# Kernel tuning notes

Measured on AMD Instinct MI355X. Metric: run time of the kernel, lower is better.

Reference implementation:

```python
import jax, jax.numpy as jnp
import numpy as np

BLOCK = 8
WIN = 3
PAD = WIN - 1


def _dct_mat(b, dtype):
    # Orthonormal DCT-II matrix: D[k, n] = s_k * sqrt(2/b) * cos(pi*(2n+1)k/(2b))
    n = np.arange(b)
    k = n[:, None]
    D = np.sqrt(2.0 / b) * np.cos(np.pi * (2 * n[None, :] + 1) * k / (2 * b))
    D[0, :] *= 1.0 / np.sqrt(2.0)
    return jnp.asarray(D, dtype=dtype)


def setup_inputs() -> dict:
    key = jax.random.key(0)
    k1, k2 = jax.random.split(key)
    x = jax.random.normal(k1, (8, 64, 256, 256), dtype=jnp.float32)
    conv_w = jax.random.normal(k2, (64, 64, WIN), dtype=jnp.float32) * 0.05
    conv_b = jnp.zeros((64,), dtype=jnp.float32)
    return {"x": x, "conv_w": conv_w, "conv_b": conv_b}


def reference(x, conv_w, conv_b):
    b = BLOCK
    bsz, ch, H, W = x.shape
    nH, nW = H // b, W // b
    n = nH * nW
    D = _dct_mat(b, x.dtype)

    # blockify: (bsz, ch, n_blocks, b, b)
    blk = x.reshape(bsz, ch, nH, b, nW, b).transpose(0, 1, 2, 4, 3, 5)
    blk = blk.reshape(bsz, ch, n, b, b)

    # block 2D DCT: D @ X @ D^T
    coef = jnp.einsum('kn,bcxnm,lm->bcxkl', D, blk, D)
    coef = coef.reshape(bsz, ch, n, b * b)

    # FreqConv: causal-right-padded Conv1d over the b*b frequency axis
    y = coef.transpose(0, 2, 1, 3).reshape(bsz * n, ch, b * b)
    y = jnp.pad(y, ((0, 0), (0, 0), (0, PAD)))
    y = jax.lax.conv_general_dilated(
        y, conv_w, window_strides=(1,), padding=[(0, 0)],
        dimension_numbers=('NCH', 'OIH', 'NCH'), feature_group_count=1)
    y = y + conv_b[None, :, None]
    out_ch = y.shape[1]
    y = y.reshape(bsz, n, out_ch, b * b).transpose(0, 2, 1, 3)

    # block 2D IDCT: D^T @ X @ D
    y = y.reshape(bsz, out_ch, n, b, b)
    img = jnp.einsum('kn,bcxkl,lm->bcxnm', D, y, D)

    # deblockify back to (bsz, out_ch, H, W)
    img = img.reshape(bsz, out_ch, nH, nW, b, b).transpose(0, 1, 2, 4, 3, 5)
    return img.reshape(bsz, out_ch, H, W)
```

## Files before the change

### kernel.cpp

```cpp
#include <hip/hip_runtime.h>


#define THREADS 256
#define HW 256
#define CH 64
#define CT_ROW 72
#define CT_SAMPLE (66 * CT_ROW)
#define LDS_BYTES (4 * CT_SAMPLE * 2)

typedef __attribute__((ext_vector_type(8))) short short8b;
typedef __attribute__((ext_vector_type(8))) unsigned short us8;
typedef __attribute__((ext_vector_type(4))) float f32x4;
typedef __attribute__((ext_vector_type(4))) unsigned short us4;

__device__ inline unsigned short f2bf(float f) {
    unsigned u = __builtin_bit_cast(unsigned, f);
    u += 0x7FFFu + ((u >> 16) & 1u);
    return (unsigned short)(u >> 16);
}

__device__ __constant__ static const float D8[8][8] = {
  { 0.3535533906f, 0.3535533906f, 0.3535533906f, 0.3535533906f, 0.3535533906f, 0.3535533906f, 0.3535533906f, 0.3535533906f },
  { 0.4903926402f, 0.4157348062f, 0.2777851165f, 0.0975451610f,-0.0975451610f,-0.2777851165f,-0.4157348062f,-0.4903926402f },
  { 0.4619397663f, 0.1913417162f,-0.1913417162f,-0.4619397663f,-0.4619397663f,-0.1913417162f, 0.1913417162f, 0.4619397663f },
  { 0.4157348062f,-0.0975451610f,-0.4903926402f,-0.2777851165f, 0.2777851165f, 0.4903926402f, 0.0975451610f,-0.4157348062f },
  { 0.3535533906f,-0.3535533906f,-0.3535533906f, 0.3535533906f, 0.3535533906f,-0.3535533906f,-0.3535533906f, 0.3535533906f },
  { 0.2777851165f,-0.4903926402f, 0.0975451610f, 0.4157348062f,-0.4157348062f,-0.0975451610f, 0.4903926402f,-0.2777851165f },
  { 0.1913417162f,-0.4619397663f, 0.4619397663f,-0.1913417162f,-0.1913417162f, 0.4619397663f,-0.4619397663f, 0.1913417162f },
  { 0.0975451610f,-0.2777851165f, 0.4157348062f,-0.4903926402f, 0.4903926402f,-0.4157348062f, 0.2777851165f,-0.0975451610f },
};

__global__ __launch_bounds__(256)
void prep_kernel(const float* __restrict__ conv_w, unsigned short* __restrict__ ws16) {
    int j = blockIdx.x * 256 + threadIdx.x;
    if (j < 4096) {
        int t = j >> 6, s = j & 63;
        ws16[j] = f2bf(D8[t >> 3][s >> 3] * D8[t & 7][s & 7]);
    } else if (j < 8192) {
        int jj = j - 4096;
        int s = jj >> 6, t = jj & 63;
        ws16[j] = f2bf(D8[t >> 3][s >> 3] * D8[t & 7][s & 7]);
    } else if (j < 20480) {
        int jj = j - 8192;
        int w = jj >> 12, rem = jj & 4095, o = rem >> 6, i = rem & 63;
        ws16[j] = f2bf(conv_w[o * 192 + i * 3 + w]);
    }
}

__global__ __launch_bounds__(THREADS, 4)
void dct_freq_conv_kernel(const float* __restrict__ x,
                          const unsigned short* __restrict__ ws16,
                          const float* __restrict__ conv_b,
                          float* __restrict__ out)
{
    extern __shared__ char smem[];
    unsigned short* Ct = (unsigned short*)smem;
    const unsigned short* Trm = ws16;
    const unsigned short* Urm = ws16 + 4096;
    const unsigned short* Wt  = ws16 + 8192;

    const int tid  = threadIdx.x;
    const int wid  = tid >> 6;
    const int lane = tid & 63;
    const int lr   = lane & 15;
    const int lq   = lane >> 4;
    const int bz   = blockIdx.z;
    const int by   = blockIdx.y;
    const int bxs  = blockIdx.x * 4 + wid;

    unsigned short* CtP = Ct + wid * CT_SAMPLE;

    if (lane < 36) *(us4*)&CtP[64 * CT_ROW + lane * 4] = (us4){0, 0, 0, 0};

    float bias[4];
    #pragma unroll
    for (int m = 0; m < 4; ++m) bias[m] = conv_b[m * 16 + lr];

    #pragma unroll
    for (int mg = 0; mg < 2; ++mg) {
        f32x4 acc[2][4];
        #pragma unroll
        for (int i = 0; i < 2; ++i)
            #pragma unroll
            for (int n = 0; n < 4; ++n) acc[i][n] = (f32x4){0.f, 0.f, 0.f, 0.f};

        #pragma unroll
        for (int kc = 0; kc < 2; ++kc) {
            short8b a[2], b[4];
            #pragma unroll
            for (int mh = 0; mh < 2; ++mh) {
                const int c = (mg * 2 + mh) * 16 + lr;
                const float* xp = x + (((size_t)bz * CH + c) * HW + by * 8 + kc * 4 + lq) * HW
                                    + bxs * 8;
                float4 u0 = *(const float4*)xp;
                float4 u1 = *(const float4*)(xp + 4);
                us8 pa;
                pa[0] = f2bf(u0.x); pa[1] = f2bf(u0.y); pa[2] = f2bf(u0.z); pa[3] = f2bf(u0.w);
                pa[4] = f2bf(u1.x); pa[5] = f2bf(u1.y); pa[6] = f2bf(u1.z); pa[7] = f2bf(u1.w);
                a[mh] = __builtin_bit_cast(short8b, pa);
            }
            #pragma unroll
            for (int n = 0; n < 4; ++n)
                b[n] = *(const short8b*)&Trm[(n * 16 + lr) * 64 + kc * 32 + lq * 8];
            #pragma unroll
            for (int mh = 0; mh < 2; ++mh)
                #pragma unroll
                for (int n = 0; n < 4; ++n)
                    acc[mh][n] = __builtin_amdgcn_mfma_f32_16x16x32_bf16(
                        a[mh], b[n], acc[mh][n], 0, 0, 0);
        }
        #pragma unroll
        for (int mh = 0; mh < 2; ++mh) {
            const int c0 = (mg * 2 + mh) * 16 + lq * 4;
            #pragma unroll
            for (int n = 0; n < 4; ++n) {
                us4 pk;
                #pragma unroll
                for (int j = 0; j < 4; ++j) pk[j] = f2bf(acc[mh][n][j]);
                *(us4*)&CtP[(n * 16 + lr) * CT_ROW + c0] = pk;
            }
        }
    }

    f32x4 acc2[4][4];
    #pragma unroll
    for (int n = 0; n < 4; ++n)
        #pragma unroll
        for (int m = 0; m < 4; ++m) acc2[n][m] = (f32x4){0.f, 0.f, 0.f, 0.f};

    #pragma unroll 2
    for (int kc = 0; kc < 6; ++kc) {
        const int w  = kc >> 1;
        const int i0 = (kc & 1) * 32 + 8 * lq;
        short8b a[4], b[4];
        #pragma unroll
        for (int n = 0; n < 4; ++n)
            a[n] = *(const short8b*)&CtP[(n * 16 + lr + w) * CT_ROW + i0];
        #pragma unroll
        for (int m = 0; m < 4; ++m)
            b[m] = *(const short8b*)&Wt[(w * 64 + m * 16 + lr) * 64 + i0];
        #pragma unroll
        for (int n = 0; n < 4; ++n)
            #pragma unroll
            for (int m = 0; m < 4; ++m)
                acc2[n][m] = __builtin_amdgcn_mfma_f32_16x16x32_bf16(
                    a[n], b[m], acc2[n][m], 0, 0, 0);
    }
    #pragma unroll
    for (int n = 0; n < 4; ++n) {
        const int t0 = n * 16 + 4 * lq;
        #pragma unroll
        for (int m = 0; m < 4; ++m) {
            const int o = m * 16 + lr;
            us4 pk;
            #pragma unroll
            for (int j = 0; j < 4; ++j) pk[j] = f2bf(acc2[n][m][j] + bias[m]);
            *(us4*)&CtP[o * CT_ROW + t0] = pk;
        }
    }

    #pragma unroll
    for (int mg = 0; mg < 2; ++mg) {
        f32x4 acc[2][4];
        #pragma unroll
        for (int i = 0; i < 2; ++i)
            #pragma unroll
            for (int ct = 0; ct < 4; ++ct) acc[i][ct] = (f32x4){0.f, 0.f, 0.f, 0.f};

        #pragma unroll
        for (int kc = 0; kc < 2; ++kc) {
            short8b a[2], b[4];
            #pragma unroll
            for (int mh = 0; mh < 2; ++mh)
                a[mh] = *(const short8b*)&Urm[((mg * 2 + mh) * 16 + lr) * 64 + kc * 32 + lq * 8];
            #pragma unroll
            for (int ct = 0; ct < 4; ++ct)
                b[ct] = *(const short8b*)&CtP[(ct * 16 + lr) * CT_ROW + kc * 32 + lq * 8];
            #pragma unroll
            for (int mh = 0; mh < 2; ++mh)
                #pragma unroll
                for (int ct = 0; ct < 4; ++ct)
                    acc[mh][ct] = __builtin_amdgcn_mfma_f32_16x16x32_bf16(
                        a[mh], b[ct], acc[mh][ct], 0, 0, 0);
        }
        #pragma unroll
        for (int mh = 0; mh < 2; ++mh) {
            const int s0 = (mg * 2 + mh) * 16 + lq * 4;
            const int n  = s0 >> 3;
            const int m0 = s0 & 7;
            #pragma unroll
            for (int ct = 0; ct < 4; ++ct) {
                const int o = ct * 16 + lr;
                float4 st = make_float4(acc[mh][ct][0], acc[mh][ct][1],
                                        acc[mh][ct][2], acc[mh][ct][3]);
                *(float4*)(out + (((size_t)bz * CH + o) * HW + by * 8 + n) * HW
                           + bxs * 8 + m0) = st;
            }
        }
    }
}

extern "C" void kernel_launch(void* const* d_in, const int* in_sizes, int n_in,
                              void* d_out, int out_size, void* d_ws, size_t ws_size,
                              hipStream_t stream) {
    const float* x  = (const float*)d_in[0];
    const float* cw = (const float*)d_in[1];
    const float* cb = (const float*)d_in[2];
    float* o        = (float*)d_out;
    unsigned short* ws16 = (unsigned short*)d_ws;

    prep_kernel<<<dim3(80), dim3(256), 0, stream>>>(cw, ws16);

    hipFuncSetAttribute(reinterpret_cast<const void*>(dct_freq_conv_kernel),
                        hipFuncAttributeMaxDynamicSharedMemorySize,
                        (int)LDS_BYTES);
    dim3 grid(8, 32, 8);
    dct_freq_conv_kernel<<<grid, dim3(THREADS), LDS_BYTES, stream>>>(x, ws16, cb, o);
}
```

Before: 286.0 us.

## Stage input and output through swizzled LDS for coalesced global access

Input tiles are now loaded cooperatively by the whole block as coalesced float4 rows, converted to bf16 and written into an XOR-swizzled LDS buffer before the forward DCT GEMM. Outputs pass through LDS so each store writes contiguous 32-float row segments instead of scattered 8-float pieces per wave. The weight matrices are pre-permuted into MFMA fragment order so each lane does one contiguous load. In exchange the kernel uses more LDS, adds several block-wide barriers, and lowers the occupancy hint from 4 to 3.

```diff
diff --git a/kernel.cpp b/kernel.cpp
--- a/kernel.cpp
+++ b/kernel.cpp
@@ -6,10 +6,10 @@
 #define CH 64
 #define CT_ROW 72
 #define CT_SAMPLE (66 * CT_ROW)
-#define LDS_BYTES (4 * CT_SAMPLE * 2)
+#define XB_SH 8192
+#define LDS_BYTES ((XB_SH + 4 * CT_SAMPLE) * 2)
 
 typedef __attribute__((ext_vector_type(8))) short short8b;
-typedef __attribute__((ext_vector_type(8))) unsigned short us8;
 typedef __attribute__((ext_vector_type(4))) float f32x4;
 typedef __attribute__((ext_vector_type(4))) unsigned short us4;
 
@@ -32,42 +32,44 @@
 
 __global__ __launch_bounds__(256)
 void prep_kernel(const float* __restrict__ conv_w, unsigned short* __restrict__ ws16) {
-    int j = blockIdx.x * 256 + threadIdx.x;
-    if (j < 4096) {
-        int t = j >> 6, s = j & 63;
-        ws16[j] = f2bf(D8[t >> 3][s >> 3] * D8[t & 7][s & 7]);
-    } else if (j < 8192) {
-        int jj = j - 4096;
-        int s = jj >> 6, t = jj & 63;
-        ws16[j] = f2bf(D8[t >> 3][s >> 3] * D8[t & 7][s & 7]);
-    } else if (j < 20480) {
-        int jj = j - 8192;
-        int w = jj >> 12, rem = jj & 4095, o = rem >> 6, i = rem & 63;
-        ws16[j] = f2bf(conv_w[o * 192 + i * 3 + w]);
+    int idx = blockIdx.x * 256 + threadIdx.x;
+    int j = idx & 7, lane = (idx >> 3) & 63;
+    int lrr = lane & 15, lqq = lane >> 4;
+    if (idx < 4096) {
+        int nk = idx >> 9, n = nk >> 1, kc = nk & 1;
+        int t = n * 16 + lrr, s = kc * 32 + lqq * 8 + j;
+        ws16[idx] = f2bf(D8[t >> 3][s >> 3] * D8[t & 7][s & 7]);
+    } else if (idx < 8192) {
+        int i2 = idx - 4096;
+        int mk = i2 >> 9, m = mk >> 1, kc = mk & 1;
+        int s = m * 16 + lrr, t = kc * 32 + lqq * 8 + j;
+        ws16[idx] = f2bf(D8[t >> 3][s >> 3] * D8[t & 7][s & 7]);
+    } else if (idx < 20480) {
+        int i3 = idx - 8192;
+        int grp = i3 >> 9, m = grp & 3, hc = (grp >> 2) & 1, w = grp >> 3;
+        int o = m * 16 + lrr, i = hc * 32 + lqq * 8 + j;
+        ws16[idx] = f2bf(conv_w[o * 192 + i * 3 + w]);
     }
 }
 
-__global__ __launch_bounds__(THREADS, 4)
+__global__ __launch_bounds__(THREADS, 3)
 void dct_freq_conv_kernel(const float* __restrict__ x,
                           const unsigned short* __restrict__ ws16,
                           const float* __restrict__ conv_b,
                           float* __restrict__ out)
 {
     extern __shared__ char smem[];
-    unsigned short* Ct = (unsigned short*)smem;
-    const unsigned short* Trm = ws16;
-    const unsigned short* Urm = ws16 + 4096;
-    const unsigned short* Wt  = ws16 + 8192;
-
-    const int tid  = threadIdx.x;
-    const int wid  = tid >> 6;
-    const int lane = tid & 63;
-    const int lr   = lane & 15;
-    const int lq   = lane >> 4;
-    const int bz   = blockIdx.z;
-    const int by   = blockIdx.y;
-    const int bxs  = blockIdx.x * 4 + wid;
-
+    unsigned short* Xb = (unsigned short*)smem;
+    float*          Ou = (float*)smem;
+    unsigned short* Ct = (unsigned short*)smem + XB_SH;
+    const unsigned short* Tf = ws16;
+    const unsigned short* Uf = ws16 + 4096;
+    const unsigned short* Wf = ws16 + 8192;
+
+    const int tid = threadIdx.x;
+    const int wid = tid >> 6, lane = tid & 63;
+    const int lr = lane & 15, lq = lane >> 4;
+    const int bz = blockIdx.z, by = blockIdx.y, bx = blockIdx.x;
     unsigned short* CtP = Ct + wid * CT_SAMPLE;
 
     if (lane < 36) *(us4*)&CtP[64 * CT_ROW + lane * 4] = (us4){0, 0, 0, 0};
@@ -76,51 +78,60 @@
     #pragma unroll
     for (int m = 0; m < 4; ++m) bias[m] = conv_b[m * 16 + lr];
 
-    #pragma unroll
-    for (int mg = 0; mg < 2; ++mg) {
-        f32x4 acc[2][4];
-        #pragma unroll
-        for (int i = 0; i < 2; ++i)
-            #pragma unroll
-            for (int n = 0; n < 4; ++n) acc[i][n] = (f32x4){0.f, 0.f, 0.f, 0.f};
-
-        #pragma unroll
-        for (int kc = 0; kc < 2; ++kc) {
-            short8b a[2], b[4];
-            #pragma unroll
-            for (int mh = 0; mh < 2; ++mh) {
-                const int c = (mg * 2 + mh) * 16 + lr;
-                const float* xp = x + (((size_t)bz * CH + c) * HW + by * 8 + kc * 4 + lq) * HW
-                                    + bxs * 8;
-                float4 u0 = *(const float4*)xp;
-                float4 u1 = *(const float4*)(xp + 4);
-                us8 pa;
-                pa[0] = f2bf(u0.x); pa[1] = f2bf(u0.y); pa[2] = f2bf(u0.z); pa[3] = f2bf(u0.w);
-                pa[4] = f2bf(u1.x); pa[5] = f2bf(u1.y); pa[6] = f2bf(u1.z); pa[7] = f2bf(u1.w);
-                a[mh] = __builtin_bit_cast(short8b, pa);
-            }
+    auto stage = [&](int h) {
+        #pragma unroll
+        for (int rep = 0; rep < 8; ++rep) {
+            int f4 = rep * 256 + tid;
+            int cl = f4 & 7, rl = (f4 >> 3) & 3, c = f4 >> 5;
+            const float* gp = x + ((size_t)(bz * 64 + c) * 256 + by * 8 + h * 4 + rl) * 256
+                                + bx * 32 + cl * 4;
+            float4 v = *(const float4*)gp;
+            us4 pk; pk[0] = f2bf(v.x); pk[1] = f2bf(v.y); pk[2] = f2bf(v.z); pk[3] = f2bf(v.w);
+            int smp = cl >> 1, kk = rl * 8 + (cl & 1) * 4;
+            *(us4*)&Xb[smp * 2048 + c * 32 + (kk ^ ((c & 3) << 3))] = pk;
+        }
+    };
+
+    f32x4 acc[4][4];
+    #pragma unroll
+    for (int m = 0; m < 4; ++m)
+        #pragma unroll
+        for (int n = 0; n < 4; ++n) acc[m][n] = (f32x4){0.f, 0.f, 0.f, 0.f};
+
+    auto gemm1_step = [&](int kc) {
+        short8b a[4], b[4];
+        #pragma unroll
+        for (int m = 0; m < 4; ++m) {
+            const int cA = m * 16 + lr;
+            a[m] = *(const short8b*)&Xb[wid * 2048 + cA * 32 + ((lq * 8) ^ ((cA & 3) << 3))];
+        }
+        #pragma unroll
+        for (int n = 0; n < 4; ++n)
+            b[n] = *(const short8b*)&Tf[((n * 2 + kc) * 64 + lane) * 8];
+        #pragma unroll
+        for (int m = 0; m < 4; ++m)
             #pragma unroll
             for (int n = 0; n < 4; ++n)
-                b[n] = *(const short8b*)&Trm[(n * 16 + lr) * 64 + kc * 32 + lq * 8];
-            #pragma unroll
-            for (int mh = 0; mh < 2; ++mh)
-                #pragma unroll
-                for (int n = 0; n < 4; ++n)
-                    acc[mh][n] = __builtin_amdgcn_mfma_f32_16x16x32_bf16(
-                        a[mh], b[n], acc[mh][n], 0, 0, 0);
-        }
-        #pragma unroll
-        for (int mh = 0; mh < 2; ++mh) {
-            const int c0 = (mg * 2 + mh) * 16 + lq * 4;
-            #pragma unroll
-            for (int n = 0; n < 4; ++n) {
-                us4 pk;
-                #pragma unroll
-                for (int j = 0; j < 4; ++j) pk[j] = f2bf(acc[mh][n][j]);
-                *(us4*)&CtP[(n * 16 + lr) * CT_ROW + c0] = pk;
-            }
-        }
-    }
+                acc[m][n] = __builtin_amdgcn_mfma_f32_16x16x32_bf16(a[m], b[n], acc[m][n], 0, 0, 0);
+    };
+
+    stage(0);
+    __syncthreads();
+    gemm1_step(0);
+    __syncthreads();
+    stage(1);
+    __syncthreads();
+    gemm1_step(1);
+
+    #pragma unroll
+    for (int m = 0; m < 4; ++m)
+        #pragma unroll
+        for (int n = 0; n < 4; ++n) {
+            us4 pk;
+            #pragma unroll
+            for (int j = 0; j < 4; ++j) pk[j] = f2bf(acc[m][n][j]);
+            *(us4*)&CtP[(n * 16 + lr) * CT_ROW + m * 16 + lq * 4] = pk;
+        }
 
     f32x4 acc2[4][4];
     #pragma unroll
@@ -128,74 +139,75 @@
         #pragma unroll
         for (int m = 0; m < 4; ++m) acc2[n][m] = (f32x4){0.f, 0.f, 0.f, 0.f};
 
-    #pragma unroll 2
+    #pragma unroll
     for (int kc = 0; kc < 6; ++kc) {
         const int w  = kc >> 1;
-        const int i0 = (kc & 1) * 32 + 8 * lq;
+        const int i0 = (kc & 1) * 32 + lq * 8;
         short8b a[4], b[4];
         #pragma unroll
         for (int n = 0; n < 4; ++n)
             a[n] = *(const short8b*)&CtP[(n * 16 + lr + w) * CT_ROW + i0];
         #pragma unroll
         for (int m = 0; m < 4; ++m)
-            b[m] = *(const short8b*)&Wt[(w * 64 + m * 16 + lr) * 64 + i0];
+            b[m] = *(const short8b*)&Wf[((kc * 4 + m) * 64 + lane) * 8];
         #pragma unroll
         for (int n = 0; n < 4; ++n)
             #pragma unroll
             for (int m = 0; m < 4; ++m)
-                acc2[n][m] = __builtin_amdgcn_mfma_f32_16x16x32_bf16(
-                    a[n], b[m], acc2[n][m], 0, 0, 0);
+                acc2[n][m] = __builtin_amdgcn_mfma_f32_16x16x32_bf16(a[n], b[m], acc2[n][m], 0, 0, 0);
     }
     #pragma unroll
-    for (int n = 0; n < 4; ++n) {
-        const int t0 = n * 16 + 4 * lq;
+    for (int n = 0; n < 4; ++n)
         #pragma unroll
         for (int m = 0; m < 4; ++m) {
-            const int o = m * 16 + lr;
             us4 pk;
             #pragma unroll
             for (int j = 0; j < 4; ++j) pk[j] = f2bf(acc2[n][m][j] + bias[m]);
-            *(us4*)&CtP[o * CT_ROW + t0] = pk;
-        }
-    }
+            *(us4*)&CtP[(m * 16 + lr) * CT_ROW + n * 16 + lq * 4] = pk;
+        }
 
     #pragma unroll
     for (int mg = 0; mg < 2; ++mg) {
-        f32x4 acc[2][4];
-        #pragma unroll
-        for (int i = 0; i < 2; ++i)
-            #pragma unroll
-            for (int ct = 0; ct < 4; ++ct) acc[i][ct] = (f32x4){0.f, 0.f, 0.f, 0.f};
+        f32x4 a3[2][4];
+        #pragma unroll
+        for (int mh = 0; mh < 2; ++mh)
+            #pragma unroll
+            for (int ct = 0; ct < 4; ++ct) a3[mh][ct] = (f32x4){0.f, 0.f, 0.f, 0.f};
 
         #pragma unroll
         for (int kc = 0; kc < 2; ++kc) {
-            short8b a[2], b[4];
+            short8b ua[2], yb[4];
             #pragma unroll
             for (int mh = 0; mh < 2; ++mh)
-                a[mh] = *(const short8b*)&Urm[((mg * 2 + mh) * 16 + lr) * 64 + kc * 32 + lq * 8];
+                ua[mh] = *(const short8b*)&Uf[(((mg * 2 + mh) * 2 + kc) * 64 + lane) * 8];
             #pragma unroll
             for (int ct = 0; ct < 4; ++ct)
-                b[ct] = *(const short8b*)&CtP[(ct * 16 + lr) * CT_ROW + kc * 32 + lq * 8];
+                yb[ct] = *(const short8b*)&CtP[(ct * 16 + lr) * CT_ROW + kc * 32 + lq * 8];
             #pragma unroll
             for (int mh = 0; mh < 2; ++mh)
                 #pragma unroll
                 for (int ct = 0; ct < 4; ++ct)
-                    acc[mh][ct] = __builtin_amdgcn_mfma_f32_16x16x32_bf16(
-                        a[mh], b[ct], acc[mh][ct], 0, 0, 0);
-        }
+                    a3[mh][ct] = __builtin_amdgcn_mfma_f32_16x16x32_bf16(ua[mh], yb[ct], a3[mh][ct], 0, 0, 0);
+        }
+
         #pragma unroll
         for (int mh = 0; mh < 2; ++mh) {
-            const int s0 = (mg * 2 + mh) * 16 + lq * 4;
-            const int n  = s0 >> 3;
-            const int m0 = s0 & 7;
-            #pragma unroll
-            for (int ct = 0; ct < 4; ++ct) {
-                const int o = ct * 16 + lr;
-                float4 st = make_float4(acc[mh][ct][0], acc[mh][ct][1],
-                                        acc[mh][ct][2], acc[mh][ct][3]);
-                *(float4*)(out + (((size_t)bz * CH + o) * HW + by * 8 + n) * HW
-                           + bxs * 8 + m0) = st;
+            const int q = mg * 2 + mh;
+            #pragma unroll
+            for (int ct = 0; ct < 4; ++ct)
+                *(f32x4*)&Ou[wid * 1024 + (ct * 16 + lr) * 16 + ((lq ^ wid) & 3) * 4] = a3[mh][ct];
+            __syncthreads();
+            #pragma unroll
+            for (int rep = 0; rep < 4; ++rep) {
+                int gl = tid & 1, smp = (tid >> 1) & 3, c = (rep & 1) * 32 + (tid >> 3);
+                int gh = rep >> 1, g = gh * 2 + gl;
+                f32x4 v = *(const f32x4*)&Ou[smp * 1024 + c * 16 + ((g ^ smp) & 3) * 4];
+                int r = q * 2 + gh;
+                *(float4*)(out + ((size_t)(bz * 64 + c) * 256 + by * 8 + r) * 256
+                           + bx * 32 + smp * 8 + gl * 4)
+                    = make_float4(v[0], v[1], v[2], v[3]);
             }
+            __syncthreads();
         }
     }
 }
```

Result: faster. 258.4 us (-9.6%).
